# Performance work log

Measured on AMD Instinct MI355X. Metric: run time of the kernel, lower is better.

## Reference

```python
import jax, jax.numpy as jnp
import numpy as np
from jax import lax


def _l2n(t, eps=1e-12):
    n = jnp.sqrt(jnp.sum(t * t, axis=-1, keepdims=True))
    return t / jnp.maximum(n, eps)


def _ln(t, w, b, eps=1e-5):
    mu = jnp.mean(t, -1, keepdims=True)
    var = jnp.var(t, -1, keepdims=True)
    return (t - mu) / jnp.sqrt(var + eps) * w + b


def _unfold3(x):
    # nn.Unfold(kernel_size=3, padding=1, stride=1): [B,C,H,W] -> [B,C,9,H*W]
    B, C, H, W = x.shape
    xp = jnp.pad(x, ((0, 0), (0, 0), (1, 1), (1, 1)))
    pat = jnp.stack([xp[:, :, i:i + H, j:j + W] for i in range(3) for j in range(3)], axis=2)
    return pat.reshape(B, C, 9, H * W)


def _forward(x, norm1_w, norm1_b, q_w, q_b, kv_w, kv_b, temperature, query_embedding,
             learnable_tokens, learnable_bias, sr_w, sr_b, pln_w, pln_b, proj_w, proj_b,
             norm2_w, norm2_b, fc1_w, fc1_b, dw_w, dw_b, fc2_w, fc2_b):
    B, C, H, W = x.shape
    nh = temperature.shape[0]
    d = C // nh
    N = H * W
    K = 9  # local_len = window_size**2
    # norm1 (WithBias LayerNorm over channel dim, channels-last)
    y = _ln(x.reshape(B, C, N).transpose(0, 2, 1), norm1_w, norm1_b)  # [B,N,C]
    # ---- AggregatedAttention ----
    q = (y @ q_w.T + q_b).reshape(B, N, nh, d).transpose(0, 2, 1, 3)  # [B,h,N,d]
    qn = _l2n(q)
    qs = (qn + query_embedding) * jax.nn.softplus(temperature)
    kv = y @ kv_w.T + kv_b  # [B,N,2C]
    k_loc = _l2n(kv[..., :C].reshape(B, N, nh, d)).reshape(B, N, C)
    kvl = jnp.concatenate([k_loc, kv[..., C:]], -1).transpose(0, 2, 1).reshape(B, 2 * C, H, W)
    pat = _unfold3(kvl).reshape(B, 2 * nh, d, K, N).transpose(0, 1, 4, 2, 3)  # [B,2h,N,d,K]
    k_l, v_l = pat[:, :nh], pat[:, nh:]
    attn_local = jnp.einsum('bhnd,bhndk->bhnk', qs, k_l)  # [B,h,N,K]
    # pooled branch; sr_ratio=1 so adaptive_avg_pool2d is identity
    y4 = y.transpose(0, 2, 1).reshape(B, C, H, W)
    xp = jax.nn.gelu(jnp.einsum('oc,bchw->bohw', sr_w, y4) + sr_b[:, None, None], approximate=False)
    xp = _ln(xp.reshape(B, C, N).transpose(0, 2, 1), pln_w, pln_b)  # [B,pool_len,C]
    kvp = (xp @ kv_w.T + kv_b).reshape(B, N, 2 * nh, d).transpose(0, 2, 1, 3)
    k_p = _l2n(kvp[:, :nh])
    v_p = kvp[:, nh:]
    attn_pool = jnp.einsum('bhnd,bhmd->bhnm', qs, k_p)  # [B,h,N,pool_len]
    attn = jax.nn.softmax(jnp.concatenate([attn_local, attn_pool], -1), axis=-1)
    a_l, a_p = attn[..., :K], attn[..., K:]
    w_l = jnp.einsum('bhnd,hdk->bhnk', qn, learnable_tokens) + learnable_bias + a_l
    x_local = jnp.einsum('bhnk,bhndk->bhnd', w_l, v_l)
    x_pool = jnp.einsum('bhnm,bhmd->bhnd', a_p, v_p)
    xo = (x_local + x_pool).transpose(0, 2, 1, 3).reshape(B, N, C)
    # proj then raw torch-style reshape [B,N,C] -> [B,C,H,W] (memory reinterpretation)
    xo = (xo @ proj_w.T + proj_b).reshape(B, C, H, W)
    x = x + xo
    # ---- ConvolutionalGLU MLP ----
    hf = dw_b.shape[0]
    y2 = _ln(x.reshape(B, C, N).transpose(0, 2, 1), norm2_w, norm2_b).transpose(0, 2, 1).reshape(B, C, H, W)
    f1 = jnp.einsum('oc,bchw->bohw', fc1_w, y2) + fc1_b[:, None, None]
    a, v = f1[:, :hf], f1[:, hf:]
    dw = lax.conv_general_dilated(a, dw_w, (1, 1), ((1, 1), (1, 1)),
                                  feature_group_count=hf,
                                  dimension_numbers=('NCHW', 'OIHW', 'NCHW')) + dw_b[:, None, None]
    g = jax.nn.gelu(dw, approximate=False) * v
    out = jnp.einsum('oc,bchw->bohw', fc2_w, g) + fc2_b[:, None, None]
    return x + out


def setup_inputs() -> dict:
    key = jax.random.key(0)
    B, C, H, W = 2, 128, 56, 56
    nh, d, K = 4, 32, 9
    hf = int(2 * int(C * 4.0) / 3)  # 341
    ks = iter(jax.random.split(key, 16))
    rn = lambda shape, s=0.02: jax.random.normal(next(ks), shape, jnp.float32) * s
    return {
        'x': jax.random.normal(next(ks), (B, C, H, W), jnp.float32),
        'norm1_w': jnp.ones((C,), jnp.float32), 'norm1_b': jnp.zeros((C,), jnp.float32),
        'q_w': rn((C, C)), 'q_b': jnp.zeros((C,), jnp.float32),
        'kv_w': rn((2 * C, C)), 'kv_b': jnp.zeros((2 * C,), jnp.float32),
        'temperature': jnp.full((nh, 1, 1), float(np.log(np.exp(1.0 / 0.24) - 1.0)), jnp.float32),
        'query_embedding': rn((nh, 1, d)),
        'learnable_tokens': rn((nh, d, K)),
        'learnable_bias': jnp.zeros((nh, 1, K), jnp.float32),
        'sr_w': rn((C, C)), 'sr_b': jnp.zeros((C,), jnp.float32),
        'pln_w': jnp.ones((C,), jnp.float32), 'pln_b': jnp.zeros((C,), jnp.float32),
        'proj_w': rn((C, C)), 'proj_b': jnp.zeros((C,), jnp.float32),
        'norm2_w': jnp.ones((C,), jnp.float32), 'norm2_b': jnp.zeros((C,), jnp.float32),
        'fc1_w': rn((2 * hf, C)), 'fc1_b': jnp.zeros((2 * hf,), jnp.float32),
        'dw_w': rn((hf, 1, 3, 3)), 'dw_b': jnp.zeros((hf,), jnp.float32),
        'fc2_w': rn((C, hf)), 'fc2_b': jnp.zeros((C,), jnp.float32),
    }


def reference(x, norm1_w, norm1_b, q_w, q_b, kv_w, kv_b, temperature, query_embedding,
              learnable_tokens, learnable_bias, sr_w, sr_b, pln_w, pln_b, proj_w, proj_b,
              norm2_w, norm2_b, fc1_w, fc1_b, dw_w, dw_b, fc2_w, fc2_b):
    return _forward(x, norm1_w, norm1_b, q_w, q_b, kv_w, kv_b, temperature, query_embedding,
                    learnable_tokens, learnable_bias, sr_w, sr_b, pln_w, pln_b, proj_w, proj_b,
                    norm2_w, norm2_b, fc1_w, fc1_b, dw_w, dw_b, fc2_w, fc2_b)
```

## Files before the change

kernel.cpp:

```cpp
#include <hip/hip_runtime.h>
#include <hip/hip_bf16.h>

typedef __hip_bfloat16 bf16;
typedef short s8v __attribute__((ext_vector_type(8)));
typedef short s4v __attribute__((ext_vector_type(4)));
typedef float f4v __attribute__((ext_vector_type(4)));

#define DEVI __device__ __forceinline__

DEVI float cvt(float x){ return x; }
DEVI float cvt(bf16 x){ return __bfloat162float(x); }

DEVI void stg(float* p, float v){ *p = v; }
DEVI void stg(bf16* p, float v){ *p = __float2bfloat16(v); }

DEVI float gelu_exact(float x){
  return 0.5f*x*(1.0f + erff(x*0.70710678118654752440f));
}

constexpr int B_ = 2, C_ = 128, H_ = 56, W_ = 56, N_ = 3136, NH_ = 4, D_ = 32, HF_ = 341;
constexpr int ROWS_ = B_*N_;
constexpr int KF2 = 352;
constexpr int GQ_ = NH_*B_*N_;
constexpr int FW = 512;
constexpr int KSP = 8;
constexpr int SPLIT = 384;
constexpr float LOG2E = 1.4426950408889634f;
constexpr float E8L2  = 11.541560327111707f;

template<typename TX, typename TY, bool PLANES>
__global__ __launch_bounds__(256)
void ln_kernel(const TX* __restrict__ x, long xstr, const float* __restrict__ w,
               const float* __restrict__ bia, TY* __restrict__ y)
{
  int gid = blockIdx.x*4 + (threadIdx.x>>6);
  int lane = threadIdx.x & 63;
  int b = gid / N_, n = gid % N_;
  float v0, v1;
  if (PLANES){
    v0 = cvt(x[((long)b*C_ + lane     )*N_ + n]);
    v1 = cvt(x[((long)b*C_ + lane + 64)*N_ + n]);
  } else {
    v0 = cvt(x[(long)gid*xstr + lane     ]);
    v1 = cvt(x[(long)gid*xstr + lane + 64]);
  }
  float s = v0+v1, ss = v0*v0 + v1*v1;
  #pragma unroll
  for (int o=32;o>0;o>>=1){ s += __shfl_xor(s,o); ss += __shfl_xor(ss,o); }
  float mu  = s*(1.0f/128.0f);
  float var = fmaxf(ss*(1.0f/128.0f) - mu*mu, 0.f);
  float inv = rsqrtf(var + 1e-5f);
  stg(&y[(long)gid*C_ + lane     ], (v0-mu)*inv*w[lane     ] + bia[lane     ]);
  stg(&y[(long)gid*C_ + lane + 64], (v1-mu)*inv*w[lane + 64] + bia[lane + 64]);
}

__global__ __launch_bounds__(256)
void convw_kernel(const float* __restrict__ q_w, const float* __restrict__ kv_w,
                  const float* __restrict__ sr_w, const float* __restrict__ proj_w,
                  const float* __restrict__ fc1_w, const float* __restrict__ fc2_w,
                  const float* __restrict__ q_b, const float* __restrict__ kv_b,
                  const float* __restrict__ sr_b,
                  bf16* __restrict__ out, float* __restrict__ bias_out)
{
  int t = blockIdx.x*256 + threadIdx.x;
  if (t >= 214272){
    int i = t - 214272;
    if (i < 512){
      float bv = (i < 128) ? q_b[i] : (i < 384) ? kv_b[i-128] : sr_b[i-384];
      bias_out[i] = bv;
    }
    return;
  }
  float v;
  if      (t <  16384) v = q_w[t];
  else if (t <  49152) v = kv_w[t-16384];
  else if (t <  65536) v = sr_w[t-49152];
  else if (t <  81920) v = proj_w[t-65536];
  else if (t < 169216) v = fc1_w[t-81920];
  else {
    int i = t - 169216; int m = i / KF2, kp = i % KF2;
    v = (kp < HF_) ? fc2_w[m*HF_ + kp] : 0.f;
  }
  out[t] = __float2bfloat16(v);
}

template<int KT, int MODE, typename TC>
__global__ __launch_bounds__(256)
void gemm_mfma(const bf16* __restrict__ A, const bf16* __restrict__ B,
               const float* __restrict__ bias, const float* __restrict__ res,
               TC* __restrict__ Cm, int M, int Nn,
               long sA, long sB, long sC, long sR,
               const float* __restrict__ qe, const float* __restrict__ temp,
               bf16* __restrict__ aux0, bf16* __restrict__ aux1)
{
  A  += (long)blockIdx.z * sA;
  B  += (long)blockIdx.z * sB;
  Cm += (long)blockIdx.z * sC;
  if (res) res += (long)blockIdx.z * sR;
  int lane = threadIdx.x & 63, w = threadIdx.x >> 6;
  int m = lane & 15, quad = lane >> 4;
  int n0 = blockIdx.x*64, m0 = blockIdx.y*64;
  int arow = m0 + w*16 + m;
  if (arow >= M) arow = M-1;
  const bf16* ap = A + (long)arow*KT + quad*8;
  const bf16* bp = B + (long)(n0 + m)*KT + quad*8;
  f4v acc[4];
  #pragma unroll
  for (int s=0;s<4;s++) acc[s] = (f4v){0.f,0.f,0.f,0.f};
  #pragma unroll
  for (int k0 = 0; k0 < KT; k0 += 32){
    s8v af = *(const s8v*)(ap + k0);
    #pragma unroll
    for (int s=0;s<4;s++){
      s8v bf = *(const s8v*)(bp + (long)s*16*KT + k0);
      acc[s] = __builtin_amdgcn_mfma_f32_16x16x32_bf16(af, bf, acc[s], 0, 0, 0);
    }
  }
  if ((MODE==6 || MODE==7) && blockIdx.x < 2){
    int hA = blockIdx.x*2, hB = hA+1;
    float spA = 0.f, spB = 0.f;
    if (MODE==6){
      spA = log1pf(expf(temp[hA])) * LOG2E;
      spB = log1pf(expf(temp[hB])) * LOG2E;
    }
    #pragma unroll
    for (int r=0;r<4;r++){
      float v4[4];
      #pragma unroll
      for (int s=0;s<4;s++) v4[s] = acc[s][r] + bias[n0 + s*16 + m];
      float ssA = v4[0]*v4[0] + v4[1]*v4[1];
      float ssB = v4[2]*v4[2] + v4[3]*v4[3];
      #pragma unroll
      for (int off=1; off<16; off<<=1){
        ssA += __shfl_xor(ssA, off);
        ssB += __shfl_xor(ssB, off);
      }
      float invA = 1.f/fmaxf(sqrtf(ssA), 1e-12f);
      float invB = 1.f/fmaxf(sqrtf(ssB), 1e-12f);
      int gm = m0 + w*16 + quad*4 + r;
      int b = gm / N_, n = gm % N_;
      #pragma unroll
      for (int s=0;s<4;s++){
        int h = (s<2) ? hA : hB;
        int d = (s&1)*16 + m;
        float v = v4[s] * ((s<2) ? invA : invB);
        if (MODE==6) v = (v + qe[h*D_ + d]) * ((s<2) ? spA : spB);
        aux0[((long)(b*NH_+h)*N_ + n)*D_ + d] = __float2bfloat16(v);
      }
    }
    return;
  }
  if (MODE==7){
    int gm0 = m0 + w*16 + quad*4;
    int b = gm0 / N_, nb = gm0 % N_;
    #pragma unroll
    for (int s=0;s<4;s++){
      int h = (blockIdx.x-2)*2 + (s>>1);
      int d = (s&1)*16 + m;
      bf16 p4[4];
      #pragma unroll
      for (int r=0;r<4;r++) p4[r] = __float2bfloat16(acc[s][r] + bias[n0 + s*16 + m]);
      *(s4v*)(aux1 + ((long)(b*NH_+h)*D_ + d)*N_ + nb) = *(const s4v*)p4;
    }
    return;
  }
  #pragma unroll
  for (int s=0;s<4;s++){
    int gn = n0 + s*16 + m;
    #pragma unroll
    for (int r=0;r<4;r++){
      int gm = m0 + w*16 + quad*4 + r;
      if (gm >= M) continue;
      float v = acc[s][r];
      if (MODE==1 || MODE==4 || MODE==6) v += bias[gn];
      else                               v += bias[gm];
      if (MODE==6 && gn >= 384) v = gelu_exact(v);
      if (MODE==4 || MODE==5) v += res[(long)gm*Nn + gn];
      stg(&Cm[(long)gm*Nn + gn], v);
    }
  }
}

__global__ __launch_bounds__(256)
void attn_part_kernel(const bf16* __restrict__ qs_, const bf16* __restrict__ kp_,
                      const bf16* __restrict__ vp_,
                      bf16* __restrict__ Op, float* __restrict__ Lp)
{
  int bh = blockIdx.y;
  int z  = blockIdx.z;
  int lane = threadIdx.x & 63;
  int w    = threadIdx.x >> 6;
  int m    = lane & 15, quad = lane >> 4;
  int base = blockIdx.x*256 + w*16;
  __shared__ float sm[4][2304];
  bf16*  Pl   = (bf16*)sm[w];
  float* Olds = sm[w];

  s8v af[4]; bool hasQ[4];
  #pragma unroll
  for (int ch=0; ch<4; ch++){
    int qq = base + ch*64;
    hasQ[ch] = (qq < N_);
    af[ch] = *(const s8v*)(qs_ + ((long)bh*N_ + (hasQ[ch] ? qq : base) + m)*D_ + quad*8);
  }
  const bf16* kpb = kp_ + (long)bh*N_*D_;
  const bf16* vpb = vp_ + (long)bh*D_*N_;
  f4v o0[4], o1[4];
  float l[4];
  #pragma unroll
  for (int ch=0; ch<4; ch++){
    o0[ch] = (f4v){0.f,0.f,0.f,0.f}; o1[ch] = (f4v){0.f,0.f,0.f,0.f};
    l[ch] = 0.f;
  }

  int tlo = z*SPLIT, thi = (z==KSP-1) ? N_ : tlo + SPLIT;
  for (int t0 = tlo; t0 < thi; t0 += 64){
    s8v kf[4], vf[4];
    #pragma unroll
    for (int s=0;s<4;s++)
      kf[s] = *(const s8v*)(kpb + (long)(t0 + s*16 + m)*D_ + quad*8);
    vf[0] = *(const s8v*)(vpb + (long)(m     )*N_ + t0      + quad*8);
    vf[1] = *(const s8v*)(vpb + (long)(16 + m)*N_ + t0      + quad*8);
    vf[2] = *(const s8v*)(vpb + (long)(m     )*N_ + t0 + 32 + quad*8);
    vf[3] = *(const s8v*)(vpb + (long)(16 + m)*N_ + t0 + 32 + quad*8);
    #pragma unroll
    for (int s = 0; s < 4; s++){
      #pragma unroll
      for (int ch=0; ch<4; ch++){
        f4v c = {-E8L2, -E8L2, -E8L2, -E8L2};
        c = __builtin_amdgcn_mfma_f32_16x16x32_bf16(kf[s], af[ch], c, 0, 0, 0);
        bf16 p4[4];
        float e0 = __builtin_amdgcn_exp2f(c[0]);
        float e1 = __builtin_amdgcn_exp2f(c[1]);
        float e2 = __builtin_amdgcn_exp2f(c[2]);
        float e3 = __builtin_amdgcn_exp2f(c[3]);
        l[ch] += (e0+e1) + (e2+e3);
        p4[0] = __float2bfloat16(e0); p4[1] = __float2bfloat16(e1);
        p4[2] = __float2bfloat16(e2); p4[3] = __float2bfloat16(e3);
        *(s4v*)(Pl + ch*1152 + m*72 + s*16 + quad*4) = *(const s4v*)p4;
      }
    }
    #pragma unroll
    for (int c2=0;c2<2;c2++){
      #pragma unroll
      for (int ch=0; ch<4; ch++){
        s8v pa = *(const s8v*)(Pl + ch*1152 + m*72 + c2*32 + quad*8);
        o0[ch] = __builtin_amdgcn_mfma_f32_16x16x32_bf16(pa, vf[c2*2  ], o0[ch], 0, 0, 0);
        o1[ch] = __builtin_amdgcn_mfma_f32_16x16x32_bf16(pa, vf[c2*2+1], o1[ch], 0, 0, 0);
      }
    }
  }
  #pragma unroll
  for (int ch=0; ch<4; ch++){
    if (!hasQ[ch]) continue;
    float lr = l[ch];
    lr += __shfl_xor(lr, 16);
    lr += __shfl_xor(lr, 32);
    #pragma unroll
    for (int r=0;r<4;r++){
      Olds[(quad*4+r)*36 + m     ] = o0[ch][r];
      Olds[(quad*4+r)*36 + 16 + m] = o1[ch][r];
    }
    long gq = (long)bh*N_ + base + ch*64 + m;
    f4v ov0 = *(const f4v*)(Olds + m*36 + quad*8);
    f4v ov1 = *(const f4v*)(Olds + m*36 + quad*8 + 4);
    bf16 o8[8];
    #pragma unroll
    for (int j=0;j<4;j++){ o8[j] = __float2bfloat16(ov0[j]); o8[4+j] = __float2bfloat16(ov1[j]); }
    *(s8v*)(Op + ((long)z*GQ_ + gq)*32 + quad*8) = *(const s8v*)o8;
    if (quad == 0) Lp[(long)z*GQ_ + gq] = lr;
  }
}

__global__ __launch_bounds__(256)
void attn_combine_kernel(const bf16* __restrict__ Op, const float* __restrict__ Lp,
                         const bf16* __restrict__ qs_, const bf16* __restrict__ fused,
                         const float* __restrict__ qe, const float* __restrict__ temp,
                         const float* __restrict__ tokens, const float* __restrict__ tbias,
                         bf16* __restrict__ xo)
{
  int gq = blockIdx.x*256 + threadIdx.x;
  int n = gq % N_; int bh = gq / N_; int h = bh & 3; int b = bh >> 2;
  float L = 0.f;
  float out[32];
  #pragma unroll
  for (int d=0;d<32;d++) out[d] = 0.f;
  #pragma unroll
  for (int z=0; z<KSP; z++){
    L += Lp[(long)z*GQ_ + gq];
    const bf16* oz = Op + ((long)z*GQ_ + gq)*32;
    #pragma unroll
    for (int d=0;d<32;d++) out[d] += cvt(oz[d]);
  }
  const bf16* qrow = qs_ + (long)gq*D_;
  float q[32];
  #pragma unroll
  for (int d=0;d<32;d++) q[d] = cvt(qrow[d]) * 0.6931471805599453f;
  int hy = n / W_, wx = n % W_;
  const bf16* kvb = fused + (long)b*N_*FW + 128 + h*D_;
  float sl[9];
  #pragma unroll
  for (int k=0;k<9;k++){
    int di = k/3-1, dj = k%3-1;
    int yy = hy+di, xx = wx+dj;
    float s = 0.f;
    if (yy>=0 && yy<H_ && xx>=0 && xx<W_){
      long nn2 = (long)(yy*W_+xx)*FW;
      float dot = 0.f, ss = 0.f;
      #pragma unroll
      for (int d=0;d<32;d++){
        float kk = cvt(kvb[nn2 + d]);
        dot = fmaf(q[d], kk, dot);
        ss  = fmaf(kk, kk, ss);
      }
      s = dot / fmaxf(sqrtf(ss), 1e-12f);
    }
    sl[k] = s;
  }
  #pragma unroll
  for (int k=0;k<9;k++) L += __expf(sl[k] - 8.f);
  float invL = 1.f/L;
  #pragma unroll
  for (int d=0;d<32;d++) out[d] *= invL;
  float sp = log1pf(expf(temp[h]));
  float invsp = 1.f/sp;
  float qn[32];
  #pragma unroll
  for (int d=0;d<32;d++) qn[d] = q[d]*invsp - qe[h*D_+d];
  #pragma unroll
  for (int k=0;k<9;k++){
    float tok = 0.f;
    #pragma unroll
    for (int d=0;d<32;d++) tok = fmaf(qn[d], tokens[(h*D_+d)*9+k], tok);
    float wl = tok + tbias[h*9+k] + __expf(sl[k] - 8.f)*invL;
    int di = k/3-1, dj = k%3-1;
    int yy = hy+di, xx = wx+dj;
    if (yy>=0 && yy<H_ && xx>=0 && xx<W_){
      long nn2 = (long)(yy*W_+xx)*FW;
      #pragma unroll
      for (int d=0;d<32;d++) out[d] = fmaf(wl, cvt(kvb[nn2 + 128 + d]), out[d]);
    }
  }
  bf16* op = xo + ((long)(b*N_ + n))*C_ + h*D_;
  #pragma unroll
  for (int d=0;d<32;d++) stg(&op[d], out[d]);
}

__global__ __launch_bounds__(256)
void dwconv_kernel(const bf16* __restrict__ f1, const float* __restrict__ dww,
                   const float* __restrict__ dwb, bf16* __restrict__ g)
{
  int t = blockIdx.x*256 + threadIdx.x;
  if (t >= B_*N_*44) return;
  int b = t / (N_*44); int r = t - b*(N_*44);
  int n = r % N_, cg = r / N_;
  f1 += (long)b*2*HF_*N_;
  g  += (long)b*N_*KF2;
  int c0 = cg*8;
  int hy = n / W_, wx = n % W_;
  bf16 o8[8];
  #pragma unroll
  for (int j=0;j<8;j++){
    int c = c0 + j;
    float val = 0.f;
    if (c < HF_){
      const bf16* ap = f1 + (long)c*N_;
      float s = dwb[c];
      #pragma unroll
      for (int di=-1; di<=1; di++)
        #pragma unroll
        for (int dj=-1; dj<=1; dj++){
          int yy = hy+di, xx = wx+dj;
          if (yy>=0 && yy<H_ && xx>=0 && xx<W_)
            s = fmaf(dww[c*9 + (di+1)*3 + (dj+1)], cvt(ap[yy*W_+xx]), s);
        }
      val = gelu_exact(s) * cvt(f1[(long)(HF_+c)*N_ + n]);
    }
    o8[j] = __float2bfloat16(val);
  }
  *(s8v*)(g + (long)n*KF2 + c0) = *(const s8v*)o8;
}

extern "C" void kernel_launch(void* const* d_in, const int* in_sizes, int n_in,
                              void* d_out, int out_size, void* d_ws, size_t ws_size,
                              hipStream_t stream)
{
  (void)in_sizes; (void)n_in; (void)out_size; (void)ws_size;
  const float* x_in      = (const float*)d_in[0];
  const float* norm1_w   = (const float*)d_in[1];
  const float* norm1_b   = (const float*)d_in[2];
  const float* q_w       = (const float*)d_in[3];
  const float* q_b       = (const float*)d_in[4];
  const float* kv_w      = (const float*)d_in[5];
  const float* kv_b      = (const float*)d_in[6];
  const float* temp      = (const float*)d_in[7];
  const float* qe        = (const float*)d_in[8];
  const float* tokens    = (const float*)d_in[9];
  const float* tbias     = (const float*)d_in[10];
  const float* sr_w      = (const float*)d_in[11];
  const float* sr_b      = (const float*)d_in[12];
  const float* pln_w     = (const float*)d_in[13];
  const float* pln_b     = (const float*)d_in[14];
  const float* proj_w    = (const float*)d_in[15];
  const float* proj_b    = (const float*)d_in[16];
  const float* norm2_w   = (const float*)d_in[17];
  const float* norm2_b   = (const float*)d_in[18];
  const float* fc1_w     = (const float*)d_in[19];
  const float* fc1_b     = (const float*)d_in[20];
  const float* dw_w      = (const float*)d_in[21];
  const float* dw_b      = (const float*)d_in[22];
  const float* fc2_w     = (const float*)d_in[23];
  const float* fc2_b     = (const float*)d_in[24];

  char* w8 = (char*)d_ws;
  bf16*  fused   = (bf16*)(w8 + 0);
  float* x2      = (float*)(w8 + 0);
  bf16*  y2      = (bf16*)(w8 + 3211264);
  bf16*  f1b     = (bf16*)(w8 + 4816896);
  bf16*  qs      = (bf16*)(w8 + 6422528);
  bf16*  xp      = (bf16*)(w8 + 8028160);
  bf16*  k_p     = (bf16*)(w8 + 9633792);
  bf16*  v_p     = (bf16*)(w8 + 11239424);
  bf16*  Opart   = (bf16*)(w8 + 13045056);
  bf16*  g_rows  = (bf16*)(w8 + 25890112);
  bf16*  wbase   = (bf16*)(w8 + 30305600);
  float* fbias   = (float*)(w8 + 30734144);
  bf16*  y       = f1b;
  bf16*  xo      = (bf16*)d_out;
  float* Lpart   = (float*)((char*)d_out + 1605632);
  bf16*  proj_wb = wbase + 65536;
  bf16*  fc1_wb  = wbase + 81920;
  bf16*  fc2_wb  = wbase + 169216;

  convw_kernel<<<(214784+255)/256, 256, 0, stream>>>(
      q_w, kv_w, sr_w, proj_w, fc1_w, fc2_w, q_b, kv_b, sr_b, wbase, fbias);
  ln_kernel<float, bf16, true><<<ROWS_/4, 256, 0, stream>>>(x_in, 0, norm1_w, norm1_b, y);
  gemm_mfma<128, 6, bf16><<<dim3(8,98), 256, 0, stream>>>(
      y, wbase, fbias, nullptr, fused, ROWS_, FW, 0,0,0,0, qe, temp, qs, nullptr);
  ln_kernel<bf16, bf16, false><<<ROWS_/4, 256, 0, stream>>>(fused + 384, FW, pln_w, pln_b, xp);
  gemm_mfma<128, 7, bf16><<<dim3(4,98), 256, 0, stream>>>(
      xp, wbase + 16384, kv_b, nullptr, (bf16*)nullptr, ROWS_, 256, 0,0,0,0,
      nullptr, nullptr, k_p, v_p);
  attn_part_kernel<<<dim3(13,8,KSP), 256, 0, stream>>>(qs, k_p, v_p, Opart, Lpart);
  attn_combine_kernel<<<GQ_/256, 256, 0, stream>>>(Opart, Lpart, qs, fused,
                                                   qe, temp, tokens, tbias, xo);
  gemm_mfma<128, 4, float><<<dim3(2,98), 256, 0, stream>>>(
      xo, proj_wb, proj_b, x_in, x2, ROWS_, 128, 0,0,0,0, nullptr, nullptr, nullptr, nullptr);
  ln_kernel<float, bf16, true><<<ROWS_/4, 256, 0, stream>>>(x2, 0, norm2_w, norm2_b, y2);
  gemm_mfma<128, 3, bf16><<<dim3(49,11,B_), 256, 0, stream>>>(
      fc1_wb, y2, fc1_b, nullptr, f1b, 2*HF_, N_,
      0, (long)N_*C_, (long)2*HF_*N_, 0, nullptr, nullptr, nullptr, nullptr);
  dwconv_kernel<<<(B_*N_*44+255)/256, 256, 0, stream>>>(f1b, dw_w, dw_b, g_rows);
  gemm_mfma<KF2, 5, float><<<dim3(49,2,B_), 256, 0, stream>>>(
      fc2_wb, g_rows, fc2_b, x2, (float*)d_out, C_, N_,
      0, (long)N_*KF2, (long)C_*N_, (long)C_*N_, nullptr, nullptr, nullptr, nullptr);
}
```

Baseline: 251.7 us.

## Keep softmax probabilities in registers via f16 MFMA; tile plane LayerNorm through LDS

The attention kernel now stores V in fp16 and feeds the exponentiated scores straight from registers into 16x16x16 f16 MFMAs. This removes the LDS round-trip for P and shrinks the shared-memory footprint. The key split is also raised from 8 to 12 chunks to add more parallel blocks, and the planar LayerNorm now transposes 128-row tiles through LDS so global reads coalesce. The trade-offs are fp16 range and precision for V and P, and more partial outputs to combine. The LayerNorm launch drops to 49 large blocks, which may under-occupy the GPU.

```diff
diff --git a/kernel.cpp b/kernel.cpp
--- a/kernel.cpp
+++ b/kernel.cpp
@@ -2,9 +2,11 @@
 #include <hip/hip_bf16.h>
 
 typedef __hip_bfloat16 bf16;
+typedef _Float16 f16;
 typedef short s8v __attribute__((ext_vector_type(8)));
 typedef short s4v __attribute__((ext_vector_type(4)));
 typedef float f4v __attribute__((ext_vector_type(4)));
+typedef _Float16 h4v __attribute__((ext_vector_type(4)));
 
 #define DEVI __device__ __forceinline__
 
@@ -23,27 +25,20 @@
 constexpr int KF2 = 352;
 constexpr int GQ_ = NH_*B_*N_;
 constexpr int FW = 512;
-constexpr int KSP = 8;
-constexpr int SPLIT = 384;
+constexpr int KSP = 12;
+constexpr int SPLIT = 256;
 constexpr float LOG2E = 1.4426950408889634f;
 constexpr float E8L2  = 11.541560327111707f;
 
-template<typename TX, typename TY, bool PLANES>
-__global__ __launch_bounds__(256)
-void ln_kernel(const TX* __restrict__ x, long xstr, const float* __restrict__ w,
-               const float* __restrict__ bia, TY* __restrict__ y)
+template<typename TX, typename TY>
+__global__ __launch_bounds__(256)
+void ln_rows_kernel(const TX* __restrict__ x, long xstr, const float* __restrict__ w,
+                    const float* __restrict__ bia, TY* __restrict__ y)
 {
   int gid = blockIdx.x*4 + (threadIdx.x>>6);
   int lane = threadIdx.x & 63;
-  int b = gid / N_, n = gid % N_;
-  float v0, v1;
-  if (PLANES){
-    v0 = cvt(x[((long)b*C_ + lane     )*N_ + n]);
-    v1 = cvt(x[((long)b*C_ + lane + 64)*N_ + n]);
-  } else {
-    v0 = cvt(x[(long)gid*xstr + lane     ]);
-    v1 = cvt(x[(long)gid*xstr + lane + 64]);
-  }
+  float v0 = cvt(x[(long)gid*xstr + lane     ]);
+  float v1 = cvt(x[(long)gid*xstr + lane + 64]);
   float s = v0+v1, ss = v0*v0 + v1*v1;
   #pragma unroll
   for (int o=32;o>0;o>>=1){ s += __shfl_xor(s,o); ss += __shfl_xor(ss,o); }
@@ -52,6 +47,54 @@
   float inv = rsqrtf(var + 1e-5f);
   stg(&y[(long)gid*C_ + lane     ], (v0-mu)*inv*w[lane     ] + bia[lane     ]);
   stg(&y[(long)gid*C_ + lane + 64], (v1-mu)*inv*w[lane + 64] + bia[lane + 64]);
+}
+
+__global__ __launch_bounds__(256)
+void ln_planes_kernel(const float* __restrict__ x, const float* __restrict__ w,
+                      const float* __restrict__ bia, bf16* __restrict__ y)
+{
+  __shared__ float sm[128*129];
+  __shared__ float ps[2][128], pss[2][128], mu_s[128], inv_s[128];
+  int t = threadIdx.x;
+  int base = blockIdx.x*128;
+  int ro = t & 127, half = t >> 7;
+  {
+    int row = base + ro, b = row / N_, n = row % N_;
+    const float* xp_ = x + (long)b*C_*N_ + n;
+    #pragma unroll
+    for (int it=0; it<64; it++){
+      int c = it*2 + half;
+      sm[c*129 + ro] = xp_[(long)c*N_];
+    }
+  }
+  __syncthreads();
+  {
+    float s=0.f, ss=0.f;
+    #pragma unroll
+    for (int i=0;i<64;i++){
+      float v = sm[(half*64 + i)*129 + ro];
+      s += v; ss = fmaf(v,v,ss);
+    }
+    ps[half][ro] = s; pss[half][ro] = ss;
+  }
+  __syncthreads();
+  if (t < 128){
+    float s = ps[0][t]+ps[1][t], ss = pss[0][t]+pss[1][t];
+    float mu = s*(1.0f/128.0f);
+    float var = fmaxf(ss*(1.0f/128.0f) - mu*mu, 0.f);
+    mu_s[t] = mu; inv_s[t] = rsqrtf(var + 1e-5f);
+  }
+  __syncthreads();
+  {
+    int c = t & 127;
+    float wc = w[c], bc = bia[c];
+    #pragma unroll
+    for (int it=0; it<64; it++){
+      int r2 = it*2 + half;
+      float v = sm[c*129 + r2];
+      y[(long)(base+r2)*C_ + c] = __float2bfloat16((v - mu_s[r2])*inv_s[r2]*wc + bc);
+    }
+  }
 }
 
 __global__ __launch_bounds__(256)
@@ -91,7 +134,7 @@
                TC* __restrict__ Cm, int M, int Nn,
                long sA, long sB, long sC, long sR,
                const float* __restrict__ qe, const float* __restrict__ temp,
-               bf16* __restrict__ aux0, bf16* __restrict__ aux1)
+               bf16* __restrict__ aux0, f16* __restrict__ aux1)
 {
   A  += (long)blockIdx.z * sA;
   B  += (long)blockIdx.z * sB;
@@ -157,9 +200,9 @@
     for (int s=0;s<4;s++){
       int h = (blockIdx.x-2)*2 + (s>>1);
       int d = (s&1)*16 + m;
-      bf16 p4[4];
-      #pragma unroll
-      for (int r=0;r<4;r++) p4[r] = __float2bfloat16(acc[s][r] + bias[n0 + s*16 + m]);
+      f16 p4[4];
+      #pragma unroll
+      for (int r=0;r<4;r++) p4[r] = (f16)(acc[s][r] + bias[n0 + s*16 + m]);
       *(s4v*)(aux1 + ((long)(b*NH_+h)*D_ + d)*N_ + nb) = *(const s4v*)p4;
     }
     return;
@@ -183,7 +226,7 @@
 
 __global__ __launch_bounds__(256)
 void attn_part_kernel(const bf16* __restrict__ qs_, const bf16* __restrict__ kp_,
-                      const bf16* __restrict__ vp_,
+                      const f16* __restrict__ vp_,
                       bf16* __restrict__ Op, float* __restrict__ Lp)
 {
   int bh = blockIdx.y;
@@ -192,8 +235,7 @@
   int w    = threadIdx.x >> 6;
   int m    = lane & 15, quad = lane >> 4;
   int base = blockIdx.x*256 + w*16;
-  __shared__ float sm[4][2304];
-  bf16*  Pl   = (bf16*)sm[w];
+  __shared__ float sm[4][640];
   float* Olds = sm[w];
 
   s8v af[4]; bool hasQ[4];
@@ -204,7 +246,7 @@
     af[ch] = *(const s8v*)(qs_ + ((long)bh*N_ + (hasQ[ch] ? qq : base) + m)*D_ + quad*8);
   }
   const bf16* kpb = kp_ + (long)bh*N_*D_;
-  const bf16* vpb = vp_ + (long)bh*D_*N_;
+  const f16*  vpb = vp_ + (long)bh*D_*N_;
   f4v o0[4], o1[4];
   float l[4];
   #pragma unroll
@@ -215,38 +257,30 @@
 
   int tlo = z*SPLIT, thi = (z==KSP-1) ? N_ : tlo + SPLIT;
   for (int t0 = tlo; t0 < thi; t0 += 64){
-    s8v kf[4], vf[4];
+    s8v kf[4];
     #pragma unroll
     for (int s=0;s<4;s++)
       kf[s] = *(const s8v*)(kpb + (long)(t0 + s*16 + m)*D_ + quad*8);
-    vf[0] = *(const s8v*)(vpb + (long)(m     )*N_ + t0      + quad*8);
-    vf[1] = *(const s8v*)(vpb + (long)(16 + m)*N_ + t0      + quad*8);
-    vf[2] = *(const s8v*)(vpb + (long)(m     )*N_ + t0 + 32 + quad*8);
-    vf[3] = *(const s8v*)(vpb + (long)(16 + m)*N_ + t0 + 32 + quad*8);
+    h4v vf0[4], vf1[4];
+    #pragma unroll
+    for (int s=0;s<4;s++){
+      vf0[s] = *(const h4v*)(vpb + (long)(m     )*N_ + t0 + s*16 + quad*4);
+      vf1[s] = *(const h4v*)(vpb + (long)(16 + m)*N_ + t0 + s*16 + quad*4);
+    }
     #pragma unroll
     for (int s = 0; s < 4; s++){
       #pragma unroll
       for (int ch=0; ch<4; ch++){
         f4v c = {-E8L2, -E8L2, -E8L2, -E8L2};
         c = __builtin_amdgcn_mfma_f32_16x16x32_bf16(kf[s], af[ch], c, 0, 0, 0);
-        bf16 p4[4];
         float e0 = __builtin_amdgcn_exp2f(c[0]);
         float e1 = __builtin_amdgcn_exp2f(c[1]);
         float e2 = __builtin_amdgcn_exp2f(c[2]);
         float e3 = __builtin_amdgcn_exp2f(c[3]);
         l[ch] += (e0+e1) + (e2+e3);
-        p4[0] = __float2bfloat16(e0); p4[1] = __float2bfloat16(e1);
-        p4[2] = __float2bfloat16(e2); p4[3] = __float2bfloat16(e3);
-        *(s4v*)(Pl + ch*1152 + m*72 + s*16 + quad*4) = *(const s4v*)p4;
-      }
-    }
-    #pragma unroll
-    for (int c2=0;c2<2;c2++){
-      #pragma unroll
-      for (int ch=0; ch<4; ch++){
-        s8v pa = *(const s8v*)(Pl + ch*1152 + m*72 + c2*32 + quad*8);
-        o0[ch] = __builtin_amdgcn_mfma_f32_16x16x32_bf16(pa, vf[c2*2  ], o0[ch], 0, 0, 0);
-        o1[ch] = __builtin_amdgcn_mfma_f32_16x16x32_bf16(pa, vf[c2*2+1], o1[ch], 0, 0, 0);
+        h4v p; p[0] = (f16)e0; p[1] = (f16)e1; p[2] = (f16)e2; p[3] = (f16)e3;
+        o0[ch] = __builtin_amdgcn_mfma_f32_16x16x16f16(p, vf0[s], o0[ch], 0, 0, 0);
+        o1[ch] = __builtin_amdgcn_mfma_f32_16x16x16f16(p, vf1[s], o1[ch], 0, 0, 0);
       }
     }
   }
@@ -420,11 +454,11 @@
   bf16*  qs      = (bf16*)(w8 + 6422528);
   bf16*  xp      = (bf16*)(w8 + 8028160);
   bf16*  k_p     = (bf16*)(w8 + 9633792);
-  bf16*  v_p     = (bf16*)(w8 + 11239424);
+  f16*   v_p     = (f16*) (w8 + 11239424);
   bf16*  Opart   = (bf16*)(w8 + 13045056);
-  bf16*  g_rows  = (bf16*)(w8 + 25890112);
-  bf16*  wbase   = (bf16*)(w8 + 30305600);
-  float* fbias   = (float*)(w8 + 30734144);
+  bf16*  g_rows  = (bf16*)(w8 + 32312640);
+  bf16*  wbase   = (bf16*)(w8 + 36728128);
+  float* fbias   = (float*)(w8 + 37156672);
   bf16*  y       = f1b;
   bf16*  xo      = (bf16*)d_out;
   float* Lpart   = (float*)((char*)d_out + 1605632);
@@ -434,10 +468,10 @@
 
   convw_kernel<<<(214784+255)/256, 256, 0, stream>>>(
       q_w, kv_w, sr_w, proj_w, fc1_w, fc2_w, q_b, kv_b, sr_b, wbase, fbias);
-  ln_kernel<float, bf16, true><<<ROWS_/4, 256, 0, stream>>>(x_in, 0, norm1_w, norm1_b, y);
+  ln_planes_kernel<<<49, 256, 0, stream>>>(x_in, norm1_w, norm1_b, y);
   gemm_mfma<128, 6, bf16><<<dim3(8,98), 256, 0, stream>>>(
       y, wbase, fbias, nullptr, fused, ROWS_, FW, 0,0,0,0, qe, temp, qs, nullptr);
-  ln_kernel<bf16, bf16, false><<<ROWS_/4, 256, 0, stream>>>(fused + 384, FW, pln_w, pln_b, xp);
+  ln_rows_kernel<bf16, bf16><<<ROWS_/4, 256, 0, stream>>>(fused + 384, FW, pln_w, pln_b, xp);
   gemm_mfma<128, 7, bf16><<<dim3(4,98), 256, 0, stream>>>(
       xp, wbase + 16384, kv_b, nullptr, (bf16*)nullptr, ROWS_, 256, 0,0,0,0,
       nullptr, nullptr, k_p, v_p);
@@ -446,7 +480,7 @@
                                                    qe, temp, tokens, tbias, xo);
   gemm_mfma<128, 4, float><<<dim3(2,98), 256, 0, stream>>>(
       xo, proj_wb, proj_b, x_in, x2, ROWS_, 128, 0,0,0,0, nullptr, nullptr, nullptr, nullptr);
-  ln_kernel<float, bf16, true><<<ROWS_/4, 256, 0, stream>>>(x2, 0, norm2_w, norm2_b, y2);
+  ln_planes_kernel<<<49, 256, 0, stream>>>(x2, norm2_w, norm2_b, y2);
   gemm_mfma<128, 3, bf16><<<dim3(49,11,B_), 256, 0, stream>>>(
       fc1_wb, y2, fc1_b, nullptr, f1b, 2*HF_, N_,
       0, (long)N_*C_, (long)2*HF_*N_, 0, nullptr, nullptr, nullptr, nullptr);
```

Result: slower. 258.5 us (+2.7%).

## Feed softmax probabilities directly into fp16 MFMA, skipping LDS round-trip

Applied to the files above, without the earlier changes.

The pooled-attention kernel no longer writes exponentiated scores to shared memory and reloads them as MFMA operands. The 16x16 score tile's accumulator layout is instead reused directly as the A operand of a 16x16x16 fp16 MFMA, with V stored in fp16 by the kv GEMM epilogue. This removes LDS traffic and the associated waits and frees shared memory. The key-split count is also raised from 8 to 12 with smaller chunks to add parallelism, which grows the partial-output buffers and required shifting workspace offsets. fp16 probabilities and V trade range for mantissa precision, and the larger split count makes the combine step do more work.

```diff
diff --git a/kernel.cpp b/kernel.cpp
--- a/kernel.cpp
+++ b/kernel.cpp
@@ -2,9 +2,11 @@
 #include <hip/hip_bf16.h>
 
 typedef __hip_bfloat16 bf16;
+typedef _Float16 f16;
 typedef short s8v __attribute__((ext_vector_type(8)));
 typedef short s4v __attribute__((ext_vector_type(4)));
 typedef float f4v __attribute__((ext_vector_type(4)));
+typedef _Float16 h4v __attribute__((ext_vector_type(4)));
 
 #define DEVI __device__ __forceinline__
 
@@ -23,8 +25,8 @@
 constexpr int KF2 = 352;
 constexpr int GQ_ = NH_*B_*N_;
 constexpr int FW = 512;
-constexpr int KSP = 8;
-constexpr int SPLIT = 384;
+constexpr int KSP = 12;
+constexpr int SPLIT = 256;
 constexpr float LOG2E = 1.4426950408889634f;
 constexpr float E8L2  = 11.541560327111707f;
 
@@ -91,7 +93,7 @@
                TC* __restrict__ Cm, int M, int Nn,
                long sA, long sB, long sC, long sR,
                const float* __restrict__ qe, const float* __restrict__ temp,
-               bf16* __restrict__ aux0, bf16* __restrict__ aux1)
+               bf16* __restrict__ aux0, f16* __restrict__ aux1)
 {
   A  += (long)blockIdx.z * sA;
   B  += (long)blockIdx.z * sB;
@@ -157,9 +159,9 @@
     for (int s=0;s<4;s++){
       int h = (blockIdx.x-2)*2 + (s>>1);
       int d = (s&1)*16 + m;
-      bf16 p4[4];
-      #pragma unroll
-      for (int r=0;r<4;r++) p4[r] = __float2bfloat16(acc[s][r] + bias[n0 + s*16 + m]);
+      f16 p4[4];
+      #pragma unroll
+      for (int r=0;r<4;r++) p4[r] = (f16)(acc[s][r] + bias[n0 + s*16 + m]);
       *(s4v*)(aux1 + ((long)(b*NH_+h)*D_ + d)*N_ + nb) = *(const s4v*)p4;
     }
     return;
@@ -183,7 +185,7 @@
 
 __global__ __launch_bounds__(256)
 void attn_part_kernel(const bf16* __restrict__ qs_, const bf16* __restrict__ kp_,
-                      const bf16* __restrict__ vp_,
+                      const f16* __restrict__ vp_,
                       bf16* __restrict__ Op, float* __restrict__ Lp)
 {
   int bh = blockIdx.y;
@@ -192,8 +194,7 @@
   int w    = threadIdx.x >> 6;
   int m    = lane & 15, quad = lane >> 4;
   int base = blockIdx.x*256 + w*16;
-  __shared__ float sm[4][2304];
-  bf16*  Pl   = (bf16*)sm[w];
+  __shared__ float sm[4][640];
   float* Olds = sm[w];
 
   s8v af[4]; bool hasQ[4];
@@ -204,7 +205,7 @@
     af[ch] = *(const s8v*)(qs_ + ((long)bh*N_ + (hasQ[ch] ? qq : base) + m)*D_ + quad*8);
   }
   const bf16* kpb = kp_ + (long)bh*N_*D_;
-  const bf16* vpb = vp_ + (long)bh*D_*N_;
+  const f16*  vpb = vp_ + (long)bh*D_*N_;
   f4v o0[4], o1[4];
   float l[4];
   #pragma unroll
@@ -215,38 +216,30 @@
 
   int tlo = z*SPLIT, thi = (z==KSP-1) ? N_ : tlo + SPLIT;
   for (int t0 = tlo; t0 < thi; t0 += 64){
-    s8v kf[4], vf[4];
+    s8v kf[4];
     #pragma unroll
     for (int s=0;s<4;s++)
       kf[s] = *(const s8v*)(kpb + (long)(t0 + s*16 + m)*D_ + quad*8);
-    vf[0] = *(const s8v*)(vpb + (long)(m     )*N_ + t0      + quad*8);
-    vf[1] = *(const s8v*)(vpb + (long)(16 + m)*N_ + t0      + quad*8);
-    vf[2] = *(const s8v*)(vpb + (long)(m     )*N_ + t0 + 32 + quad*8);
-    vf[3] = *(const s8v*)(vpb + (long)(16 + m)*N_ + t0 + 32 + quad*8);
+    h4v vf0[4], vf1[4];
+    #pragma unroll
+    for (int s=0;s<4;s++){
+      vf0[s] = *(const h4v*)(vpb + (long)(m     )*N_ + t0 + s*16 + quad*4);
+      vf1[s] = *(const h4v*)(vpb + (long)(16 + m)*N_ + t0 + s*16 + quad*4);
+    }
     #pragma unroll
     for (int s = 0; s < 4; s++){
       #pragma unroll
       for (int ch=0; ch<4; ch++){
         f4v c = {-E8L2, -E8L2, -E8L2, -E8L2};
         c = __builtin_amdgcn_mfma_f32_16x16x32_bf16(kf[s], af[ch], c, 0, 0, 0);
-        bf16 p4[4];
         float e0 = __builtin_amdgcn_exp2f(c[0]);
         float e1 = __builtin_amdgcn_exp2f(c[1]);
         float e2 = __builtin_amdgcn_exp2f(c[2]);
         float e3 = __builtin_amdgcn_exp2f(c[3]);
         l[ch] += (e0+e1) + (e2+e3);
-        p4[0] = __float2bfloat16(e0); p4[1] = __float2bfloat16(e1);
-        p4[2] = __float2bfloat16(e2); p4[3] = __float2bfloat16(e3);
-        *(s4v*)(Pl + ch*1152 + m*72 + s*16 + quad*4) = *(const s4v*)p4;
-      }
-    }
-    #pragma unroll
-    for (int c2=0;c2<2;c2++){
-      #pragma unroll
-      for (int ch=0; ch<4; ch++){
-        s8v pa = *(const s8v*)(Pl + ch*1152 + m*72 + c2*32 + quad*8);
-        o0[ch] = __builtin_amdgcn_mfma_f32_16x16x32_bf16(pa, vf[c2*2  ], o0[ch], 0, 0, 0);
-        o1[ch] = __builtin_amdgcn_mfma_f32_16x16x32_bf16(pa, vf[c2*2+1], o1[ch], 0, 0, 0);
+        h4v p; p[0] = (f16)e0; p[1] = (f16)e1; p[2] = (f16)e2; p[3] = (f16)e3;
+        o0[ch] = __builtin_amdgcn_mfma_f32_16x16x16f16(p, vf0[s], o0[ch], 0, 0, 0);
+        o1[ch] = __builtin_amdgcn_mfma_f32_16x16x16f16(p, vf1[s], o1[ch], 0, 0, 0);
       }
     }
   }
@@ -420,11 +413,11 @@
   bf16*  qs      = (bf16*)(w8 + 6422528);
   bf16*  xp      = (bf16*)(w8 + 8028160);
   bf16*  k_p     = (bf16*)(w8 + 9633792);
-  bf16*  v_p     = (bf16*)(w8 + 11239424);
+  f16*   v_p     = (f16*) (w8 + 11239424);
   bf16*  Opart   = (bf16*)(w8 + 13045056);
-  bf16*  g_rows  = (bf16*)(w8 + 25890112);
-  bf16*  wbase   = (bf16*)(w8 + 30305600);
-  float* fbias   = (float*)(w8 + 30734144);
+  bf16*  g_rows  = (bf16*)(w8 + 32312640);
+  bf16*  wbase   = (bf16*)(w8 + 36728128);
+  float* fbias   = (float*)(w8 + 37156672);
   bf16*  y       = f1b;
   bf16*  xo      = (bf16*)d_out;
   float* Lpart   = (float*)((char*)d_out + 1605632);
```

Result: slower. 258.0 us (+2.5%).
